# Optimization experiments

Hardware: AMD Instinct MI355X
Metric: run time of the kernel (lower is better)

The kernel has to match this reference:

```python
import jax, jax.numpy as jnp
import numpy as np

IGNORE_INDEX = -100
N, H, V = 4096, 4096, 32000


def setup_inputs() -> dict:
    key = jax.random.key(0)
    k1, k2, k3 = jax.random.split(key, 3)
    x = jax.random.normal(k1, (N, H), dtype=jnp.float32)
    y = jax.random.randint(k2, (N,), 0, V, dtype=jnp.int64)
    # lm_head weight, torch Linear layout [out_features=V, in_features=H]
    W = jax.random.normal(k3, (V, H), dtype=jnp.float32) * (1.0 / np.sqrt(H))
    return {"x": x, "y": y, "W": W}


def reference(x, y, W):
    # Fused linear + cross-entropy, reduction='mean' over non-ignored tokens.
    logits = jnp.einsum("nh,vh->nv", x, W)            # [N, V]
    logp = jax.nn.log_softmax(logits, axis=-1)         # [N, V]
    safe_y = jnp.where(y == IGNORE_INDEX, 0, y)
    nll = -jnp.take_along_axis(logp, safe_y[:, None], axis=-1)[:, 0]  # [N]
    valid = (y != IGNORE_INDEX).astype(logits.dtype)
    n_valid = jnp.maximum(valid.sum(), 1.0)
    return (nll * valid).sum() / n_valid
```

## Files before the change

kernel.cpp:

```cpp
#include <hip/hip_runtime.h>
#include <stdint.h>
#include <math.h>

#define N_TOK 4096
#define H_DIM 4096
#define V_DIM 32000

#define BM2 256
#define BN2 256
#define BK2 128
#define NKT2 (H_DIM / BK2)
#define CT2 (V_DIM / BN2)
#define MT2 (N_TOK / BM2)
#define WSCALE 16.0f
#define WSCALE_INV 0.0625f

#define BM 128
#define BN 128
#define BK 64
#define CT_NUM (V_DIM / BN)
#define MT_NUM (N_TOK / BM)

typedef __attribute__((ext_vector_type(8))) short short8;
typedef __attribute__((ext_vector_type(4))) float f32x4;
typedef __attribute__((ext_vector_type(2))) long long2_t;

#define MFMA16(a, b, c) __builtin_amdgcn_mfma_f32_16x16x32_bf16(a, b, c, 0, 0, 0)
#define MFMAF8(a, b, c) __builtin_amdgcn_mfma_f32_16x16x32_fp8_fp8(a, b, c, 0, 0, 0)
#define BARRIER() asm volatile("s_barrier" ::: "memory")

__device__ __forceinline__ unsigned short f2bf(float x) {
  union { float f; unsigned int u; } v; v.f = x;
  unsigned int r = v.u + 0x7fffu + ((v.u >> 16) & 1u);
  return (unsigned short)(r >> 16);
}

__device__ __forceinline__ unsigned int pk4(float a, float b, float c, float d) {
  int v = __builtin_amdgcn_cvt_pk_fp8_f32(a, b, 0, false);
  v = __builtin_amdgcn_cvt_pk_fp8_f32(c, d, v, true);
  return (unsigned int)v;
}

__device__ __forceinline__ void async16(const void* g, void* lds) {
  __builtin_amdgcn_global_load_lds(
      (const __attribute__((address_space(1))) void*)g,
      (__attribute__((address_space(3))) void*)lds, 16, 0, 0);
}

__global__ __launch_bounds__(256) void cast_f32_to_fp8_k128(
    const float* __restrict__ in, uint4* __restrict__ out, long nslots,
    float scale) {
  long stride = (long)gridDim.x * blockDim.x;
  for (long slot = (long)blockIdx.x * blockDim.x + threadIdx.x; slot < nslots;
       slot += stride) {
    long b = slot >> 3;
    int s = (int)(slot & 7);
    int t = s >> 2, g = s & 3;
    const float* p0 = in + b * 128 + t * 64 + g * 8;
    const float* p1 = p0 + 32;
    float4 a0 = *(const float4*)p0, a1 = *(const float4*)(p0 + 4);
    float4 c0 = *(const float4*)p1, c1 = *(const float4*)(p1 + 4);
    uint4 o;
    o.x = pk4(a0.x * scale, a0.y * scale, a0.z * scale, a0.w * scale);
    o.y = pk4(a1.x * scale, a1.y * scale, a1.z * scale, a1.w * scale);
    o.z = pk4(c0.x * scale, c0.y * scale, c0.z * scale, c0.w * scale);
    o.w = pk4(c1.x * scale, c1.y * scale, c1.z * scale, c1.w * scale);
    out[slot] = o;
  }
}

__device__ __forceinline__ void stage8(const uint8_t* __restrict__ base,
                                       int off, char* dest, int tid) {
  async16(base + off, dest + (tid >> 6) * 1024);
}

__device__ __forceinline__ long2_t ldq(const char* base, int off) {
  return *(const long2_t*)(base + off);
}

#define CLUSTER32(MB, A0, A1, A2, A3, BB)                                   \
  do {                                                                       \
    _Pragma("unroll")                                                        \
    for (int nf = 0; nf < 4; nf++)                                           \
      acc[MB][nf] = MFMAF8(A0[0], BB[nf][0], acc[MB][nf]);                   \
    _Pragma("unroll")                                                        \
    for (int nf = 0; nf < 4; nf++)                                           \
      acc[MB + 1][nf] = MFMAF8(A1[0], BB[nf][0], acc[MB + 1][nf]);           \
    _Pragma("unroll")                                                        \
    for (int nf = 0; nf < 4; nf++)                                           \
      acc[MB + 2][nf] = MFMAF8(A2[0], BB[nf][0], acc[MB + 2][nf]);           \
    _Pragma("unroll")                                                        \
    for (int nf = 0; nf < 4; nf++)                                           \
      acc[MB + 3][nf] = MFMAF8(A3[0], BB[nf][0], acc[MB + 3][nf]);           \
    _Pragma("unroll")                                                        \
    for (int nf = 0; nf < 4; nf++)                                           \
      acc[MB][nf] = MFMAF8(A0[1], BB[nf][1], acc[MB][nf]);                   \
    _Pragma("unroll")                                                        \
    for (int nf = 0; nf < 4; nf++)                                           \
      acc[MB + 1][nf] = MFMAF8(A1[1], BB[nf][1], acc[MB + 1][nf]);           \
    _Pragma("unroll")                                                        \
    for (int nf = 0; nf < 4; nf++)                                           \
      acc[MB + 2][nf] = MFMAF8(A2[1], BB[nf][1], acc[MB + 2][nf]);           \
    _Pragma("unroll")                                                        \
    for (int nf = 0; nf < 4; nf++)                                           \
      acc[MB + 3][nf] = MFMAF8(A3[1], BB[nf][1], acc[MB + 3][nf]);           \
  } while (0)

template<int AP, int BR>
__device__ __forceinline__ void tile_fp8(char* lds,
    const uint8_t* __restrict__ Xbase, const uint8_t* __restrict__ Wbase,
    int roff, int ktA, int ktB, int tid,
    int aRowBase, int bRowBase, int c0, int c1, f32x4 (&acc)[8][4]) {
  const char* aB = lds + AP * 32768;
  char* aN = lds + (AP ^ 1) * 32768;
  const char* bB = lds + 65536 + BR * 32768;
  char* bN = lds + 65536 + ((BR + 2) % 3) * 32768;
  const int kA = ktA * 128, kB = ktB * 128;
  long2_t bb[4];

  stage8(Xbase, roff + kA,              aN + 0,    tid);
  stage8(Xbase, roff + 64 * H_DIM + kA, aN + 8192, tid);
#pragma unroll
  for (int nf = 0; nf < 4; nf++) bb[nf] = ldq(bB, bRowBase + nf * 2048 + c0);
  {
    long2_t a0 = ldq(aB, aRowBase + 0 + c0);
    long2_t a1 = ldq(aB, aRowBase + 2048 + c0);
    long2_t a2 = ldq(aB, aRowBase + 4096 + c0);
    long2_t a3 = ldq(aB, aRowBase + 6144 + c0);
    BARRIER();
    __builtin_amdgcn_s_setprio(1);
    CLUSTER32(0, a0, a1, a2, a3, bb);
    __builtin_amdgcn_s_setprio(0);
    BARRIER();
  }
  stage8(Xbase, roff + 128 * H_DIM + kA, aN + 16384, tid);
  stage8(Xbase, roff + 192 * H_DIM + kA, aN + 24576, tid);
  {
    long2_t a0 = ldq(aB, aRowBase + 8192 + c0);
    long2_t a1 = ldq(aB, aRowBase + 10240 + c0);
    long2_t a2 = ldq(aB, aRowBase + 12288 + c0);
    long2_t a3 = ldq(aB, aRowBase + 14336 + c0);
    BARRIER();
    __builtin_amdgcn_s_setprio(1);
    CLUSTER32(4, a0, a1, a2, a3, bb);
    __builtin_amdgcn_s_setprio(0);
    BARRIER();
  }
  stage8(Wbase, roff + kB,              bN + 0,    tid);
  stage8(Wbase, roff + 64 * H_DIM + kB, bN + 8192, tid);
#pragma unroll
  for (int nf = 0; nf < 4; nf++) bb[nf] = ldq(bB, bRowBase + nf * 2048 + c1);
  {
    long2_t a0 = ldq(aB, aRowBase + 0 + c1);
    long2_t a1 = ldq(aB, aRowBase + 2048 + c1);
    long2_t a2 = ldq(aB, aRowBase + 4096 + c1);
    long2_t a3 = ldq(aB, aRowBase + 6144 + c1);
    BARRIER();
    __builtin_amdgcn_s_setprio(1);
    CLUSTER32(0, a0, a1, a2, a3, bb);
    __builtin_amdgcn_s_setprio(0);
    BARRIER();
  }
  stage8(Wbase, roff + 128 * H_DIM + kB, bN + 16384, tid);
  stage8(Wbase, roff + 192 * H_DIM + kB, bN + 24576, tid);
  {
    long2_t a0 = ldq(aB, aRowBase + 8192 + c1);
    long2_t a1 = ldq(aB, aRowBase + 10240 + c1);
    long2_t a2 = ldq(aB, aRowBase + 12288 + c1);
    long2_t a3 = ldq(aB, aRowBase + 14336 + c1);
    asm volatile("s_waitcnt vmcnt(4)" ::: "memory");
    BARRIER();
    __builtin_amdgcn_s_setprio(1);
    CLUSTER32(4, a0, a1, a2, a3, bb);
    __builtin_amdgcn_s_setprio(0);
    BARRIER();
  }
}

__global__ __launch_bounds__(512, 2) void gemm_lse8(
    const uint8_t* __restrict__ Xq, const uint8_t* __restrict__ Wq,
    float* __restrict__ pmax, float* __restrict__ psum) {
  extern __shared__ char lds[];
  const int tid = threadIdx.x;
  const int lane = tid & 63;
  const int wid = tid >> 6;
  const int wm = wid >> 2, wn = wid & 3;

  int logical = (blockIdx.x & 7) * (CT2 * MT2 / 8) + (blockIdx.x >> 3);
  const int ct = logical / MT2, mt = logical - ct * MT2;
  const int mbase = mt * BM2, cbase = ct * BN2;
  const uint8_t* Xbase = Xq + (size_t)mbase * H_DIM;
  const uint8_t* Wbase = Wq + (size_t)cbase * H_DIM;

  const int roff = (tid >> 3) * H_DIM + ((((tid & 7) ^ ((tid >> 3) & 7))) << 4);

  const int g2 = lane >> 4;
  const int c0 = ((g2 ^ (lane & 7)) << 4);
  const int c1 = (((4 + g2) ^ (lane & 7)) << 4);
  const int aRowBase = (wm * 128 + (lane & 15)) * 128;
  const int bRowBase = (wn * 64 + (lane & 15)) * 128;

  f32x4 acc[8][4];
#pragma unroll
  for (int i = 0; i < 8; i++)
#pragma unroll
    for (int j = 0; j < 4; j++) { f32x4 z = {0.f, 0.f, 0.f, 0.f}; acc[i][j] = z; }

  stage8(Wbase, roff + 0,            lds + 65536 + 0,     tid);
  stage8(Wbase, roff + 64 * H_DIM,   lds + 65536 + 8192,  tid);
  stage8(Wbase, roff + 128 * H_DIM,  lds + 65536 + 16384, tid);
  stage8(Wbase, roff + 192 * H_DIM,  lds + 65536 + 24576, tid);
  stage8(Xbase, roff + 0,            lds + 0,     tid);
  stage8(Xbase, roff + 64 * H_DIM,   lds + 8192,  tid);
  stage8(Xbase, roff + 128 * H_DIM,  lds + 16384, tid);
  stage8(Xbase, roff + 192 * H_DIM,  lds + 24576, tid);
  stage8(Wbase, roff + 128,               lds + 98304 + 0,     tid);
  stage8(Wbase, roff + 64 * H_DIM + 128,  lds + 98304 + 8192,  tid);
  stage8(Wbase, roff + 128 * H_DIM + 128, lds + 98304 + 16384, tid);
  stage8(Wbase, roff + 192 * H_DIM + 128, lds + 98304 + 24576, tid);
  asm volatile("s_waitcnt vmcnt(4)" ::: "memory");
  BARRIER();

#pragma unroll 1
  for (int i = 0; i < 5; i++) {
    int g = 6 * i;
    tile_fp8<0, 0>(lds, Xbase, Wbase, roff, g + 1, g + 2, tid,
                   aRowBase, bRowBase, c0, c1, acc);
    tile_fp8<1, 1>(lds, Xbase, Wbase, roff, g + 2, g + 3, tid,
                   aRowBase, bRowBase, c0, c1, acc);
    tile_fp8<0, 2>(lds, Xbase, Wbase, roff, g + 3, g + 4, tid,
                   aRowBase, bRowBase, c0, c1, acc);
    tile_fp8<1, 0>(lds, Xbase, Wbase, roff, g + 4, g + 5, tid,
                   aRowBase, bRowBase, c0, c1, acc);
    tile_fp8<0, 1>(lds, Xbase, Wbase, roff, g + 5, g + 6, tid,
                   aRowBase, bRowBase, c0, c1, acc);
    tile_fp8<1, 2>(lds, Xbase, Wbase, roff, g + 6, g + 7, tid,
                   aRowBase, bRowBase, c0, c1, acc);
  }
  tile_fp8<0, 0>(lds, Xbase, Wbase, roff, 31, 31, tid,
                 aRowBase, bRowBase, c0, c1, acc);
  tile_fp8<1, 1>(lds, Xbase, Wbase, roff, 31, 31, tid,
                 aRowBase, bRowBase, c0, c1, acc);

  asm volatile("s_waitcnt vmcnt(0)" ::: "memory");
  __syncthreads();

  float2* red = (float2*)lds;
#pragma unroll
  for (int mf = 0; mf < 8; mf++) {
#pragma unroll
    for (int qq = 0; qq < 4; qq++) {
      float v0 = acc[mf][0][qq] * WSCALE_INV, v1 = acc[mf][1][qq] * WSCALE_INV;
      float v2 = acc[mf][2][qq] * WSCALE_INV, v3 = acc[mf][3][qq] * WSCALE_INV;
      float mx = fmaxf(fmaxf(v0, v1), fmaxf(v2, v3));
#pragma unroll
      for (int d = 1; d < 16; d <<= 1) mx = fmaxf(mx, __shfl_xor(mx, d));
      float se = __expf(v0 - mx) + __expf(v1 - mx) + __expf(v2 - mx) + __expf(v3 - mx);
#pragma unroll
      for (int d = 1; d < 16; d <<= 1) se += __shfl_xor(se, d);
      if ((lane & 15) == 0) {
        int row = (wm << 7) + mf * 16 + (g2 << 2) + qq;
        float2 v; v.x = mx; v.y = se;
        red[row * 4 + wn] = v;
      }
    }
  }
  __syncthreads();
  if (tid < 256) {
    float M = -INFINITY, S = 0.f;
#pragma unroll
    for (int w = 0; w < 4; w++) {
      float2 rr = red[tid * 4 + w];
      float Mn = fmaxf(M, rr.x);
      S = S * __expf(M - Mn) + rr.y * __expf(rr.x - Mn);
      M = Mn;
    }
    size_t o = (size_t)ct * N_TOK + mbase + tid;
    pmax[o] = M;
    psum[o] = S;
  }
}

__global__ __launch_bounds__(256) void gemm_lse_small(
    const float* __restrict__ Xf, const float* __restrict__ Wf,
    float* __restrict__ pmax, float* __restrict__ psum) {
  __shared__ unsigned short As[BM * BK];
  __shared__ unsigned short Bs[BN * BK];
  const int ct = blockIdx.x / MT_NUM;
  const int mt = blockIdx.x % MT_NUM;
  const int mbase = mt * BM, cbase = ct * BN;
  const int tid = threadIdx.x;
  const int lane = tid & 63;
  const int wid = tid >> 6;
  const int wr = wid >> 1, wc = wid & 1;
  f32x4 acc[4][4];
#pragma unroll
  for (int i = 0; i < 4; i++)
#pragma unroll
    for (int j = 0; j < 4; j++) { f32x4 z = {0.f, 0.f, 0.f, 0.f}; acc[i][j] = z; }
  for (int ks = 0; ks < H_DIM / BK; ks++) {
    const int k0 = ks * BK;
#pragma unroll
    for (int r = 0; r < 4; r++) {
      int o = r * 4096 + wid * 1024 + lane * 16;
      int row = o >> 7;
      int kc = (o & 127) >> 1;
      const float* xs = Xf + (size_t)(mbase + row) * H_DIM + k0 + kc;
      const float* wv = Wf + (size_t)(cbase + row) * H_DIM + k0 + kc;
      float4 x0 = *(const float4*)xs, x1 = *(const float4*)(xs + 4);
      float4 w0 = *(const float4*)wv, w1 = *(const float4*)(wv + 4);
      short8 xa, wa;
      xa[0] = f2bf(x0.x); xa[1] = f2bf(x0.y); xa[2] = f2bf(x0.z); xa[3] = f2bf(x0.w);
      xa[4] = f2bf(x1.x); xa[5] = f2bf(x1.y); xa[6] = f2bf(x1.z); xa[7] = f2bf(x1.w);
      wa[0] = f2bf(w0.x); wa[1] = f2bf(w0.y); wa[2] = f2bf(w0.z); wa[3] = f2bf(w0.w);
      wa[4] = f2bf(w1.x); wa[5] = f2bf(w1.y); wa[6] = f2bf(w1.z); wa[7] = f2bf(w1.w);
      *(short8*)((char*)As + o) = xa;
      *(short8*)((char*)Bs + o) = wa;
    }
    __syncthreads();
#pragma unroll
    for (int kk = 0; kk < 2; kk++) {
      short8 a[4], b[4];
#pragma unroll
      for (int m = 0; m < 4; m++)
        a[m] = *(const short8*)((const char*)As +
                (wr * 64 + m * 16 + (lane & 15)) * 128 + kk * 64 + (lane >> 4) * 16);
#pragma unroll
      for (int n = 0; n < 4; n++)
        b[n] = *(const short8*)((const char*)Bs +
                (wc * 64 + n * 16 + (lane & 15)) * 128 + kk * 64 + (lane >> 4) * 16);
#pragma unroll
      for (int m = 0; m < 4; m++)
#pragma unroll
        for (int n = 0; n < 4; n++)
          acc[m][n] = MFMA16(a[m], b[n], acc[m][n]);
    }
    __syncthreads();
  }
  float* red = (float*)As;
  const int g = lane >> 4;
#pragma unroll
  for (int m = 0; m < 4; m++) {
#pragma unroll
    for (int q = 0; q < 4; q++) {
      float v0 = acc[m][0][q], v1 = acc[m][1][q], v2 = acc[m][2][q], v3 = acc[m][3][q];
      float mx = fmaxf(fmaxf(v0, v1), fmaxf(v2, v3));
#pragma unroll
      for (int d = 1; d < 16; d <<= 1) mx = fmaxf(mx, __shfl_xor(mx, d));
      float se = __expf(v0 - mx) + __expf(v1 - mx) + __expf(v2 - mx) + __expf(v3 - mx);
#pragma unroll
      for (int d = 1; d < 16; d <<= 1) se += __shfl_xor(se, d);
      if ((lane & 15) == 0) {
        int row = wr * 64 + m * 16 + g * 4 + q;
        red[row * 4 + wc * 2 + 0] = mx;
        red[row * 4 + wc * 2 + 1] = se;
      }
    }
  }
  __syncthreads();
  if (tid < BM) {
    float m0 = red[tid * 4 + 0], s0 = red[tid * 4 + 1];
    float m1 = red[tid * 4 + 2], s1 = red[tid * 4 + 3];
    float M = fmaxf(m0, m1);
    float S = s0 * __expf(m0 - M) + s1 * __expf(m1 - M);
    size_t o = (size_t)ct * N_TOK + mbase + tid;
    pmax[o] = M;
    psum[o] = S;
  }
}

__global__ __launch_bounds__(256) void target_logit(
    const float* __restrict__ X, const float* __restrict__ W,
    const int* __restrict__ y, float* __restrict__ tl) {
  __shared__ float red[4];
  int row = blockIdx.x;
  int lab = y[row];
  float s = 0.f;
  if (lab >= 0 && lab < V_DIM) {
    const float4* xr = (const float4*)(X + (size_t)row * H_DIM);
    const float4* wr = (const float4*)(W + (size_t)lab * H_DIM);
    for (int i = threadIdx.x; i < H_DIM / 4; i += 256) {
      float4 a = xr[i], b = wr[i];
      s += a.x * b.x + a.y * b.y + a.z * b.z + a.w * b.w;
    }
  }
#pragma unroll
  for (int o = 32; o > 0; o >>= 1) s += __shfl_down(s, o);
  if ((threadIdx.x & 63) == 0) red[threadIdx.x >> 6] = s;
  __syncthreads();
  if (threadIdx.x == 0) tl[row] = red[0] + red[1] + red[2] + red[3];
}

__global__ __launch_bounds__(256) void combine_rows(
    const float* __restrict__ pmax, const float* __restrict__ psum,
    const float* __restrict__ tl, const int* __restrict__ y,
    float* __restrict__ lossb, float* __restrict__ validb, int n_ct) {
  int row = blockIdx.x * 256 + threadIdx.x;
  if (row >= N_TOK) return;
  float M = -INFINITY, S = 0.f;
  for (int ct = 0; ct < n_ct; ct++) {
    float m = pmax[(size_t)ct * N_TOK + row];
    float s = psum[(size_t)ct * N_TOK + row];
    float Mn = fmaxf(M, m);
    S = S * __expf(M - Mn) + s * __expf(m - Mn);
    M = Mn;
  }
  bool valid = (y[row] != -100);
  lossb[row] = valid ? (M + __logf(S) - tl[row]) : 0.f;
  validb[row] = valid ? 1.f : 0.f;
}

__global__ __launch_bounds__(256) void finalize_loss(
    const float* __restrict__ lossb, const float* __restrict__ validb,
    float* __restrict__ out) {
  __shared__ float rs[4], rc[4];
  float s = 0.f, c = 0.f;
  for (int i = threadIdx.x; i < N_TOK; i += 256) { s += lossb[i]; c += validb[i]; }
#pragma unroll
  for (int o = 32; o > 0; o >>= 1) { s += __shfl_down(s, o); c += __shfl_down(c, o); }
  if ((threadIdx.x & 63) == 0) { rs[threadIdx.x >> 6] = s; rc[threadIdx.x >> 6] = c; }
  __syncthreads();
  if (threadIdx.x == 0) {
    float S = rs[0] + rs[1] + rs[2] + rs[3];
    float C = rc[0] + rc[1] + rc[2] + rc[3];
    out[0] = S / fmaxf(C, 1.f);
  }
}

extern "C" void kernel_launch(void* const* d_in, const int* in_sizes, int n_in,
                              void* d_out, int out_size, void* d_ws, size_t ws_size,
                              hipStream_t stream) {
  const float* x = (const float*)d_in[0];
  const int* y = (const int*)d_in[1];
  const float* W = (const float*)d_in[2];
  float* out = (float*)d_out;
  char* ws = (char*)d_ws;

  const size_t szWq = (size_t)V_DIM * H_DIM;
  const size_t szXq = (size_t)N_TOK * H_DIM;
  const size_t szP  = (size_t)CT_NUM * N_TOK * 4;
  const size_t szT  = (size_t)N_TOK * 4;
  const size_t needFull = szWq + szXq + 2 * szP + 3 * szT;

  bool full = (ws_size >= needFull);
  uint8_t* Wq = nullptr;
  uint8_t* Xq = nullptr;
  size_t off = 0;
  if (full) { Wq = (uint8_t*)ws; Xq = (uint8_t*)(ws + szWq); off = szWq + szXq; }
  float* pmax   = (float*)(ws + off); off += szP;
  float* psum   = (float*)(ws + off); off += szP;
  float* tl     = (float*)(ws + off); off += szT;
  float* lossb  = (float*)(ws + off); off += szT;
  float* validb = (float*)(ws + off);

  if (full) {
    cast_f32_to_fp8_k128<<<8192, 256, 0, stream>>>(
        W, (uint4*)Wq, (long)(szWq / 16), WSCALE);
    cast_f32_to_fp8_k128<<<2048, 256, 0, stream>>>(
        x, (uint4*)Xq, (long)(szXq / 16), 1.0f);
    (void)hipFuncSetAttribute((const void*)gemm_lse8,
        hipFuncAttributeMaxDynamicSharedMemorySize, 163840);
    gemm_lse8<<<CT2 * MT2, 512, 163840, stream>>>(Xq, Wq, pmax, psum);
    target_logit<<<N_TOK, 256, 0, stream>>>(x, W, y, tl);
    combine_rows<<<N_TOK / 256, 256, 0, stream>>>(pmax, psum, tl, y, lossb, validb, CT2);
  } else {
    gemm_lse_small<<<CT_NUM * MT_NUM, 256, 0, stream>>>(x, W, pmax, psum);
    target_logit<<<N_TOK, 256, 0, stream>>>(x, W, y, tl);
    combine_rows<<<N_TOK / 256, 256, 0, stream>>>(pmax, psum, tl, y, lossb, validb, CT_NUM);
  }
  finalize_loss<<<1, 256, 0, stream>>>(lossb, validb, out);
}
```

Before: 874.4 us.

## Drop per-cluster barriers and interleave A-fragment LDS loads with FP8 MFMAs

```diff
diff --git a/kernel.cpp b/kernel.cpp
--- a/kernel.cpp
+++ b/kernel.cpp
@@ -78,32 +78,25 @@
   return *(const long2_t*)(base + off);
 }
 
-#define CLUSTER32(MB, A0, A1, A2, A3, BB)                                   \
+#define PHASE_MFMA(CC)                                                       \
   do {                                                                       \
     _Pragma("unroll")                                                        \
-    for (int nf = 0; nf < 4; nf++)                                           \
-      acc[MB][nf] = MFMAF8(A0[0], BB[nf][0], acc[MB][nf]);                   \
-    _Pragma("unroll")                                                        \
-    for (int nf = 0; nf < 4; nf++)                                           \
-      acc[MB + 1][nf] = MFMAF8(A1[0], BB[nf][0], acc[MB + 1][nf]);           \
-    _Pragma("unroll")                                                        \
-    for (int nf = 0; nf < 4; nf++)                                           \
-      acc[MB + 2][nf] = MFMAF8(A2[0], BB[nf][0], acc[MB + 2][nf]);           \
-    _Pragma("unroll")                                                        \
-    for (int nf = 0; nf < 4; nf++)                                           \
-      acc[MB + 3][nf] = MFMAF8(A3[0], BB[nf][0], acc[MB + 3][nf]);           \
-    _Pragma("unroll")                                                        \
-    for (int nf = 0; nf < 4; nf++)                                           \
-      acc[MB][nf] = MFMAF8(A0[1], BB[nf][1], acc[MB][nf]);                   \
-    _Pragma("unroll")                                                        \
-    for (int nf = 0; nf < 4; nf++)                                           \
-      acc[MB + 1][nf] = MFMAF8(A1[1], BB[nf][1], acc[MB + 1][nf]);           \
-    _Pragma("unroll")                                                        \
-    for (int nf = 0; nf < 4; nf++)                                           \
-      acc[MB + 2][nf] = MFMAF8(A2[1], BB[nf][1], acc[MB + 2][nf]);           \
-    _Pragma("unroll")                                                        \
-    for (int nf = 0; nf < 4; nf++)                                           \
-      acc[MB + 3][nf] = MFMAF8(A3[1], BB[nf][1], acc[MB + 3][nf]);           \
+    for (int mp = 0; mp < 4; mp++) {                                         \
+      long2_t a0 = ldq(aB, aRowBase + (2 * mp) * 2048 + (CC));               \
+      long2_t a1 = ldq(aB, aRowBase + (2 * mp + 1) * 2048 + (CC));           \
+      _Pragma("unroll")                                                      \
+      for (int nf = 0; nf < 4; nf++)                                         \
+        acc[2 * mp][nf] = MFMAF8(a0[0], bb[nf][0], acc[2 * mp][nf]);         \
+      _Pragma("unroll")                                                      \
+      for (int nf = 0; nf < 4; nf++)                                         \
+        acc[2 * mp + 1][nf] = MFMAF8(a1[0], bb[nf][0], acc[2 * mp + 1][nf]); \
+      _Pragma("unroll")                                                      \
+      for (int nf = 0; nf < 4; nf++)                                         \
+        acc[2 * mp][nf] = MFMAF8(a0[1], bb[nf][1], acc[2 * mp][nf]);         \
+      _Pragma("unroll")                                                      \
+      for (int nf = 0; nf < 4; nf++)                                         \
+        acc[2 * mp + 1][nf] = MFMAF8(a1[1], bb[nf][1], acc[2 * mp + 1][nf]); \
+    }                                                                        \
   } while (0)
 
 template<int AP, int BR>
@@ -118,63 +111,29 @@
   const int kA = ktA * 128, kB = ktB * 128;
   long2_t bb[4];
 
-  stage8(Xbase, roff + kA,              aN + 0,    tid);
-  stage8(Xbase, roff + 64 * H_DIM + kA, aN + 8192, tid);
-#pragma unroll
-  for (int nf = 0; nf < 4; nf++) bb[nf] = ldq(bB, bRowBase + nf * 2048 + c0);
-  {
-    long2_t a0 = ldq(aB, aRowBase + 0 + c0);
-    long2_t a1 = ldq(aB, aRowBase + 2048 + c0);
-    long2_t a2 = ldq(aB, aRowBase + 4096 + c0);
-    long2_t a3 = ldq(aB, aRowBase + 6144 + c0);
-    BARRIER();
-    __builtin_amdgcn_s_setprio(1);
-    CLUSTER32(0, a0, a1, a2, a3, bb);
-    __builtin_amdgcn_s_setprio(0);
-    BARRIER();
-  }
+  stage8(Xbase, roff + kA,               aN + 0,     tid);
+  stage8(Xbase, roff + 64 * H_DIM + kA,  aN + 8192,  tid);
   stage8(Xbase, roff + 128 * H_DIM + kA, aN + 16384, tid);
   stage8(Xbase, roff + 192 * H_DIM + kA, aN + 24576, tid);
-  {
-    long2_t a0 = ldq(aB, aRowBase + 8192 + c0);
-    long2_t a1 = ldq(aB, aRowBase + 10240 + c0);
-    long2_t a2 = ldq(aB, aRowBase + 12288 + c0);
-    long2_t a3 = ldq(aB, aRowBase + 14336 + c0);
-    BARRIER();
-    __builtin_amdgcn_s_setprio(1);
-    CLUSTER32(4, a0, a1, a2, a3, bb);
-    __builtin_amdgcn_s_setprio(0);
-    BARRIER();
-  }
-  stage8(Wbase, roff + kB,              bN + 0,    tid);
-  stage8(Wbase, roff + 64 * H_DIM + kB, bN + 8192, tid);
-#pragma unroll
-  for (int nf = 0; nf < 4; nf++) bb[nf] = ldq(bB, bRowBase + nf * 2048 + c1);
-  {
-    long2_t a0 = ldq(aB, aRowBase + 0 + c1);
-    long2_t a1 = ldq(aB, aRowBase + 2048 + c1);
-    long2_t a2 = ldq(aB, aRowBase + 4096 + c1);
-    long2_t a3 = ldq(aB, aRowBase + 6144 + c1);
-    BARRIER();
-    __builtin_amdgcn_s_setprio(1);
-    CLUSTER32(0, a0, a1, a2, a3, bb);
-    __builtin_amdgcn_s_setprio(0);
-    BARRIER();
-  }
+#pragma unroll
+  for (int nf = 0; nf < 4; nf++) bb[nf] = ldq(bB, bRowBase + nf * 2048 + c0);
+  __builtin_amdgcn_s_setprio(1);
+  PHASE_MFMA(c0);
+  __builtin_amdgcn_s_setprio(0);
+  __builtin_amdgcn_sched_barrier(0);
+
+  stage8(Wbase, roff + kB,               bN + 0,     tid);
+  stage8(Wbase, roff + 64 * H_DIM + kB,  bN + 8192,  tid);
   stage8(Wbase, roff + 128 * H_DIM + kB, bN + 16384, tid);
   stage8(Wbase, roff + 192 * H_DIM + kB, bN + 24576, tid);
-  {
-    long2_t a0 = ldq(aB, aRowBase + 8192 + c1);
-    long2_t a1 = ldq(aB, aRowBase + 10240 + c1);
-    long2_t a2 = ldq(aB, aRowBase + 12288 + c1);
-    long2_t a3 = ldq(aB, aRowBase + 14336 + c1);
-    asm volatile("s_waitcnt vmcnt(4)" ::: "memory");
-    BARRIER();
-    __builtin_amdgcn_s_setprio(1);
-    CLUSTER32(4, a0, a1, a2, a3, bb);
-    __builtin_amdgcn_s_setprio(0);
-    BARRIER();
-  }
+#pragma unroll
+  for (int nf = 0; nf < 4; nf++) bb[nf] = ldq(bB, bRowBase + nf * 2048 + c1);
+  __builtin_amdgcn_s_setprio(1);
+  PHASE_MFMA(c1);
+  __builtin_amdgcn_s_setprio(0);
+  __builtin_amdgcn_sched_barrier(0);
+  asm volatile("s_waitcnt vmcnt(4)" ::: "memory");
+  BARRIER();
 }
 
 __global__ __launch_bounds__(512, 2) void gemm_lse8(
```

Measured after the change: 863.1 us. About the same (-1.3%).
